# Kernel optimization log

Measured on AMD Instinct MI355X. Metric: run time of the kernel, lower is better.

Reference implementation:

```python
import jax, jax.numpy as jnp
import numpy as np
from jax.scipy.special import erfinv

EMBED = 384
HEADS = 6
HEAD_DIM = EMBED // HEADS  # 64
N_FREQS = HEAD_DIM // 2    # 32
SEQ = 1025                 # 1 CLS + 32*32 patches
POS_DIM = 2
MIN_FREQ, MAX_FREQ = 0.1, 1000.0


def _phi(m: int) -> float:
    x = 2.0
    for _ in range(10):
        x = (1.0 + x) ** (1.0 / (m + 1.0))
    return x


def _uniform_directions(n: int, d: int) -> jnp.ndarray:
    # golden-ratio quasi-random directions, normalized (matches uniform_directions_jax)
    g = _phi(d)
    alpha = (1.0 / g) ** jnp.arange(1, d + 1, dtype=jnp.float32)
    i = jnp.arange(1, n + 1, dtype=jnp.float32)[:, None]
    z = jnp.fmod(i * alpha, 1.0)
    dirs = erfinv(2.0 * z - 1.0)
    return dirs / jnp.linalg.norm(dirs, axis=1, keepdims=True)


def _rope_freqs() -> jnp.ndarray:  # [h, F, P]
    omega = MIN_FREQ * (MAX_FREQ / MIN_FREQ) ** jnp.linspace(0.0, 1.0, N_FREQS)
    dirs = _uniform_directions(HEADS * N_FREQS, POS_DIM).reshape(HEADS, N_FREQS, POS_DIM)
    return dirs * omega.reshape(1, N_FREQS, 1)


def _coords_2d() -> jnp.ndarray:  # [S, 2], CLS at origin, patches in [-1,1]^2
    n = int(np.sqrt(SEQ - 1))  # 32
    yy, xx = jnp.meshgrid(jnp.arange(n), jnp.arange(n), indexing='ij')
    xf = xx.flatten().astype(jnp.float32) / (n - 1) * 2 - 1
    yf = yy.flatten().astype(jnp.float32) / (n - 1) * 2 - 1
    patch = jnp.stack([xf, yf], axis=1)
    return jnp.concatenate([jnp.zeros((1, 2), jnp.float32), patch], axis=0)


def _apply_rope(t_bshd, freqs_hFP, coords_SP):
    # theta: [S, h, F]
    theta = jnp.einsum('hfp,sp->shf', freqs_hFP, coords_SP)
    cos, sin = jnp.cos(theta), jnp.sin(theta)  # broadcast over batch
    x1, y1 = jnp.split(t_bshd, 2, axis=-1)     # [b,s,h,F] each
    return jnp.concatenate([x1 * cos - y1 * sin, x1 * sin + y1 * cos], axis=-1)


def setup_inputs() -> dict:
    key = jax.random.key(0)
    ks = jax.random.split(key, 6)
    scale = 1.0 / np.sqrt(EMBED)
    return {
        'x':  jax.random.normal(ks[0], (16, SEQ, EMBED), jnp.float32),
        'Wq': jax.random.normal(ks[1], (EMBED, EMBED), jnp.float32) * scale,
        'Wk': jax.random.normal(ks[2], (EMBED, EMBED), jnp.float32) * scale,
        'Wv': jax.random.normal(ks[3], (EMBED, EMBED), jnp.float32) * scale,
        'Wo': jax.random.normal(ks[4], (EMBED, EMBED), jnp.float32) * scale,
        'bo': jnp.zeros((EMBED,), jnp.float32),
    }


def reference(x, Wq, Wk, Wv, Wo, bo):
    b, s, e = x.shape
    freqs = _rope_freqs()   # constant buffers
    coords = _coords_2d()
    q = (x @ Wq).reshape(b, s, HEADS, HEAD_DIM)
    k = (x @ Wk).reshape(b, s, HEADS, HEAD_DIM)
    v = (x @ Wv).reshape(b, s, HEADS, HEAD_DIM)
    q = _apply_rope(q, freqs, coords)
    k = _apply_rope(k, freqs, coords)
    scores = jnp.einsum('blhd,bmhd->bhlm', q, k) / np.sqrt(HEAD_DIM)
    attn = jax.nn.softmax(scores, axis=-1)
    out = jnp.einsum('bhlm,bmhd->blhd', attn, v).reshape(b, s, e)
    return out @ Wo + bo
```

## Files before the change

kernel.cpp:

```cpp
#include <hip/hip_runtime.h>
#include <hip/hip_bf16.h>
#include <math.h>

#define EMBED 384
#define HEADS 6
#define HD    64
#define NF    32
#define SEQ   1025
#define SEQP  1088
#define BATCH 16
#define MTOT  (BATCH*SEQ)
#define NCHUNK 17
#define LSTRIDE 72
#define VSTR   68
#define GSTR 40

typedef __bf16 bf16x8 __attribute__((ext_vector_type(8)));
typedef __bf16 bf16x4 __attribute__((ext_vector_type(4)));
typedef float  f32x4  __attribute__((ext_vector_type(4)));
typedef short  s16x4  __attribute__((ext_vector_type(4)));

#define MFMA_BF16(A,B,C) __builtin_amdgcn_mfma_f32_16x16x32_bf16((A),(B),(C),0,0,0)
#define MFMA16(A,B,C) __builtin_amdgcn_mfma_f32_16x16x16bf16_1k((A),(B),(C),0,0,0)

__device__ __forceinline__ __bf16 f2bf(float f){
    __hip_bfloat16 h = __float2bfloat16(f);
    return *reinterpret_cast<__bf16*>(&h);
}
__device__ __forceinline__ short bfbits(float f){
    __hip_bfloat16 h = __float2bfloat16(f);
    return *reinterpret_cast<short*>(&h);
}

__global__ __launch_bounds__(256) void x_to_bf16_kernel(
    const float* __restrict__ x, __hip_bfloat16* __restrict__ xb)
{
    const int n4 = MTOT*EMBED/4;
    int i = blockIdx.x*256 + threadIdx.x;
    if (i < n4){
        float4 v = *reinterpret_cast<const float4*>(x + (size_t)i*4);
        bf16x4 b; b[0]=f2bf(v.x); b[1]=f2bf(v.y); b[2]=f2bf(v.z); b[3]=f2bf(v.w);
        *reinterpret_cast<bf16x4*>(reinterpret_cast<__bf16*>(xb) + (size_t)i*4) = b;
    }
}

__global__ __launch_bounds__(256) void transpose_w_kernel(
    const float* __restrict__ Wq, const float* __restrict__ Wk,
    const float* __restrict__ Wv, const float* __restrict__ Wo,
    __hip_bfloat16* __restrict__ Wt)
{
    __shared__ float tile[64][65];
    const int mat = blockIdx.z;
    const float* W = (mat==0)?Wq:(mat==1)?Wk:(mat==2)?Wv:Wo;
    const int k0 = blockIdx.x*64, n0 = blockIdx.y*64;
    const int c = threadIdx.x & 63, rq = threadIdx.x >> 6;
    #pragma unroll
    for (int i = 0; i < 16; ++i){
        int row = rq*16 + i;
        tile[row][c] = W[(size_t)(k0+row)*EMBED + n0 + c];
    }
    __syncthreads();
    #pragma unroll
    for (int i = 0; i < 16; ++i){
        int nr = rq*16 + i;
        Wt[((size_t)mat*EMBED + n0 + nr)*EMBED + k0 + c] = __float2bfloat16(tile[c][nr]);
    }
}

__device__ __forceinline__ float erfinv_f(float x){
    float w = -log1pf(-x*x);
    float p;
    if (w < 5.0f){
        w -= 2.5f;
        p = 2.81022636e-08f;
        p = fmaf(p, w, 3.43273939e-07f);
        p = fmaf(p, w, -3.5233877e-06f);
        p = fmaf(p, w, -4.39150654e-06f);
        p = fmaf(p, w, 0.00021858087f);
        p = fmaf(p, w, -0.00125372503f);
        p = fmaf(p, w, -0.00417768164f);
        p = fmaf(p, w, 0.246640727f);
        p = fmaf(p, w, 1.50140941f);
    } else {
        w = sqrtf(w) - 3.0f;
        p = -0.000200214257f;
        p = fmaf(p, w, 0.000100950558f);
        p = fmaf(p, w, 0.00134934322f);
        p = fmaf(p, w, -0.00367342844f);
        p = fmaf(p, w, 0.00573950773f);
        p = fmaf(p, w, -0.0076224613f);
        p = fmaf(p, w, 0.00943887047f);
        p = fmaf(p, w, 1.00167406f);
        p = fmaf(p, w, 2.83297682f);
    }
    return p * x;
}

__global__ void rope_tables_kernel(float* __restrict__ cos_t, float* __restrict__ sin_t){
    int idx = blockIdx.x * blockDim.x + threadIdx.x;
    if (idx >= SEQ*HEADS*NF) return;
    int f  = idx & (NF-1);
    int hf = idx / NF;
    int h  = hf % HEADS;
    int s  = hf / HEADS;

    double xd = 2.0;
    #pragma unroll
    for (int it = 0; it < 10; ++it) xd = cbrt(1.0 + xd);
    float a1 = (float)(1.0 / xd);
    float a2 = a1 * a1;

    float fi = (float)(h*NF + f + 1);
    float z1 = fmodf(fi * a1, 1.0f);
    float z2 = fmodf(fi * a2, 1.0f);
    float d1 = erfinv_f(2.0f*z1 - 1.0f);
    float d2 = erfinv_f(2.0f*z2 - 1.0f);
    float inv = 1.0f / sqrtf(d1*d1 + d2*d2);
    d1 *= inv; d2 *= inv;

    float omega = 0.1f * powf(10000.0f, (float)f / 31.0f);
    float fx = d1 * omega, fy = d2 * omega;

    float cx = 0.0f, cy = 0.0f;
    if (s > 0){
        int pi = s - 1;
        cx = (float)(pi & 31) / 31.0f * 2.0f - 1.0f;
        cy = (float)(pi >> 5) / 31.0f * 2.0f - 1.0f;
    }
    float theta = fx*cx + fy*cy;
    float sv, cv;
    sincosf(theta, &sv, &cv);
    cos_t[idx] = cv;
    sin_t[idx] = sv;
}

__global__ __launch_bounds__(256, 3) void qkv_rope_kernel(
    const __hip_bfloat16* __restrict__ xb_,
    const __hip_bfloat16* __restrict__ Wt,
    const float* __restrict__ cos_t,
    const float* __restrict__ sin_t,
    __hip_bfloat16* __restrict__ qbuf,
    __hip_bfloat16* __restrict__ kbuf,
    __hip_bfloat16* __restrict__ vbuf)
{
    __shared__ __align__(16) __bf16 xs[128*GSTR];
    __shared__ __align__(16) __bf16 bt[128*GSTR];
    const int tid = threadIdx.x;
    const int m0 = blockIdx.x * 128;
    const int j  = blockIdx.y;
    const __bf16* xb = reinterpret_cast<const __bf16*>(xb_);
    const __bf16* wt = reinterpret_cast<const __bf16*>(Wt);

    int soff[2], arow[2], brow[2];
    #pragma unroll
    for (int i = 0; i < 2; ++i){
        int g = tid + i*256;
        int row = g >> 2, kc = g & 3;
        soff[i] = row*GSTR + kc*8;
        int am = m0 + row; if (am > MTOT-1) am = MTOT-1;
        arow[i] = am;
        brow[i] = j*128 + row;
    }

    bf16x8 ar[2], br[2];
    #pragma unroll
    for (int i = 0; i < 2; ++i){
        int g = tid + i*256, kc = g & 3;
        ar[i] = *reinterpret_cast<const bf16x8*>(xb + (size_t)arow[i]*EMBED + kc*8);
        br[i] = *reinterpret_cast<const bf16x8*>(wt + (size_t)brow[i]*EMBED + kc*8);
    }

    const int w = tid >> 6;
    const int lane = tid & 63;
    const int quad = lane >> 4, low = lane & 15;
    const int mh = w >> 1, nh = w & 1;
    const int mw0 = m0 + mh*64;

    f32x4 acc[4][4] = {};
    for (int kb = 0; kb < 12; ++kb){
        __syncthreads();
        #pragma unroll
        for (int i = 0; i < 2; ++i){
            *reinterpret_cast<bf16x8*>(&xs[soff[i]]) = ar[i];
            *reinterpret_cast<bf16x8*>(&bt[soff[i]]) = br[i];
        }
        __syncthreads();
        if (kb < 11){
            const int k1 = (kb+1)*32;
            #pragma unroll
            for (int i = 0; i < 2; ++i){
                int g = tid + i*256, kc = g & 3;
                ar[i] = *reinterpret_cast<const bf16x8*>(xb + (size_t)arow[i]*EMBED + k1 + kc*8);
                br[i] = *reinterpret_cast<const bf16x8*>(wt + (size_t)brow[i]*EMBED + k1 + kc*8);
            }
        }
        bf16x8 af[4], bfr[4];
        #pragma unroll
        for (int mt = 0; mt < 4; ++mt)
            af[mt] = *reinterpret_cast<const bf16x8*>(&xs[(mh*64 + mt*16 + low)*GSTR + quad*8]);
        #pragma unroll
        for (int t = 0; t < 4; ++t)
            bfr[t] = *reinterpret_cast<const bf16x8*>(&bt[(nh*64 + t*16 + low)*GSTR + quad*8]);
        #pragma unroll
        for (int t = 0; t < 4; ++t)
            #pragma unroll
            for (int mt = 0; mt < 4; ++mt)
                acc[mt][t] = MFMA_BF16(af[mt], bfr[t], acc[mt][t]);
    }

    const int n64 = j*2 + nh;
    const int mat = n64 / 6;
    const int h   = n64 % 6;

    if (mat == 2){
        #pragma unroll
        for (int mt = 0; mt < 4; ++mt)
            #pragma unroll
            for (int t = 0; t < 4; ++t)
                #pragma unroll
                for (int r = 0; r < 4; ++r){
                    int m = mw0 + mt*16 + quad*4 + r;
                    if (m < MTOT){
                        int b = m / SEQ, s = m % SEQ;
                        vbuf[((size_t)(b*HEADS + h)*SEQ + s)*HD + t*16 + low] = __float2bfloat16(acc[mt][t][r]);
                    }
                }
    } else {
        __hip_bfloat16* ob = (mat == 0) ? qbuf : kbuf;
        const float qs_ = (mat == 0) ? 0.125f : 1.0f;
        #pragma unroll
        for (int mt = 0; mt < 4; ++mt)
            #pragma unroll
            for (int t = 0; t < 2; ++t)
                #pragma unroll
                for (int r = 0; r < 4; ++r){
                    int m = mw0 + mt*16 + quad*4 + r;
                    if (m < MTOT){
                        int b = m / SEQ, s = m % SEQ;
                        int f = t*16 + low;
                        float cv = cos_t[(s*HEADS + h)*NF + f];
                        float sv = sin_t[(s*HEADS + h)*NF + f];
                        float x1 = acc[mt][t][r];
                        float y1 = acc[mt][t+2][r];
                        size_t base = ((size_t)(b*HEADS + h)*SEQ + s)*HD;
                        ob[base + f]      = __float2bfloat16((x1*cv - y1*sv)*qs_);
                        ob[base + NF + f] = __float2bfloat16((x1*sv + y1*cv)*qs_);
                    }
                }
    }
}

__global__ __launch_bounds__(256) void vt_transpose_kernel(
    const __hip_bfloat16* __restrict__ v, __hip_bfloat16* __restrict__ vt)
{
    __shared__ __bf16 tileT[64*72];
    const int tid = threadIdx.x;
    const int bh = blockIdx.x;
    const int s0 = blockIdx.y * 64;
    const __bf16* vb = reinterpret_cast<const __bf16*>(v) + (size_t)bh*SEQ*HD;
    #pragma unroll
    for (int i = 0; i < 2; ++i){
        int ch = tid + i*256;
        int srow = ch >> 3, dg = ch & 7;
        int s = s0 + srow; if (s > SEQ-1) s = SEQ-1;
        bf16x8 val = *reinterpret_cast<const bf16x8*>(vb + (size_t)s*HD + dg*8);
        #pragma unroll
        for (int e = 0; e < 8; ++e)
            tileT[(dg*8 + e)*72 + srow] = val[e];
    }
    __syncthreads();
    __bf16* ot = reinterpret_cast<__bf16*>(vt) + (size_t)bh*HD*SEQP;
    #pragma unroll
    for (int i = 0; i < 2; ++i){
        int ch = tid + i*256;
        int d = ch >> 3, sg = ch & 7;
        bf16x8 val = *reinterpret_cast<const bf16x8*>(&tileT[d*72 + sg*8]);
        *reinterpret_cast<bf16x8*>(ot + (size_t)d*SEQP + s0 + sg*8) = val;
    }
}

__global__ __launch_bounds__(256, 4) void attn_kernel(
    const __hip_bfloat16* __restrict__ qbuf,
    const __hip_bfloat16* __restrict__ kbuf,
    const __hip_bfloat16* __restrict__ vtbuf,
    __hip_bfloat16* __restrict__ aout)
{
    __shared__ __align__(16) __bf16 kls[64*LSTRIDE];
    __shared__ __align__(16) __bf16 vls[64*VSTR];
    const int tid  = threadIdx.x;
    const int w    = tid >> 6;
    const int lane = tid & 63;
    const int quad = lane >> 4, low = lane & 15;
    const int id = blockIdx.x;
    const int bh = id % 96;
    const int qt = id / 96;
    const int b = bh / HEADS, h = bh % HEADS;
    const __bf16* qb = reinterpret_cast<const __bf16*>(qbuf);
    const __bf16* kb = reinterpret_cast<const __bf16*>(kbuf);
    const __bf16* vt = reinterpret_cast<const __bf16*>(vtbuf);
    const size_t base   = (size_t)bh * SEQ * HD;
    const size_t vtbase = (size_t)bh * HD * SEQP;
    const int q0 = qt*128 + w*32;

    int srow[2], sgk[2], soffk[2], soffv[2];
    #pragma unroll
    for (int i = 0; i < 2; ++i){
        int ch = tid + i*256;
        srow[i] = ch >> 3; sgk[i] = ch & 7;
        soffk[i] = srow[i]*LSTRIDE + sgk[i]*8;
        soffv[i] = srow[i]*VSTR    + sgk[i]*8;
    }

    bf16x8 bq[2][2];
    #pragma unroll
    for (int nt = 0; nt < 2; ++nt){
        int qs = q0 + nt*16 + low; if (qs > SEQ-1) qs = SEQ-1;
        #pragma unroll
        for (int ks = 0; ks < 2; ++ks)
            bq[nt][ks] = *reinterpret_cast<const bf16x8*>(qb + base + (size_t)qs*HD + ks*32 + quad*8);
    }

    bf16x8 kr[2], vr[2];
    #pragma unroll
    for (int i = 0; i < 2; ++i){
        int kk = srow[i]; if (kk > SEQ-1) kk = SEQ-1;
        kr[i] = *reinterpret_cast<const bf16x8*>(kb + base + (size_t)kk*HD + sgk[i]*8);
        vr[i] = *reinterpret_cast<const bf16x8*>(vt + vtbase + (size_t)srow[i]*SEQP + sgk[i]*8);
    }

    f32x4 o[2][4] = {};
    float l_i[2] = {0.f, 0.f};

    for (int c = 0; c < NCHUNK; ++c){
        const int c0 = c*64;
        __syncthreads();
        #pragma unroll
        for (int i = 0; i < 2; ++i){
            *reinterpret_cast<bf16x8*>(&kls[soffk[i]]) = kr[i];
            bf16x4 vlo = __builtin_shufflevector(vr[i], vr[i], 0,1,2,3);
            bf16x4 vhi = __builtin_shufflevector(vr[i], vr[i], 4,5,6,7);
            *reinterpret_cast<bf16x4*>(&vls[soffv[i]])     = vlo;
            *reinterpret_cast<bf16x4*>(&vls[soffv[i] + 4]) = vhi;
        }
        __syncthreads();
        if (c + 1 < NCHUNK){
            const int c1 = c0 + 64;
            #pragma unroll
            for (int i = 0; i < 2; ++i){
                int kk = c1 + srow[i]; if (kk > SEQ-1) kk = SEQ-1;
                kr[i] = *reinterpret_cast<const bf16x8*>(kb + base + (size_t)kk*HD + sgk[i]*8);
                vr[i] = *reinterpret_cast<const bf16x8*>(vt + vtbase + (size_t)srow[i]*SEQP + c1 + sgk[i]*8);
            }
        }
        f32x4 st[4][2] = {};
        #pragma unroll
        for (int kt = 0; kt < 4; ++kt)
            #pragma unroll
            for (int ks = 0; ks < 2; ++ks){
                bf16x8 ak = *reinterpret_cast<const bf16x8*>(&kls[(kt*16 + low)*LSTRIDE + ks*32 + quad*8]);
                #pragma unroll
                for (int nt = 0; nt < 2; ++nt)
                    st[kt][nt] = MFMA_BF16(ak, bq[nt][ks], st[kt][nt]);
            }
        if (c0 + 64 > SEQ){
            #pragma unroll
            for (int kt = 0; kt < 4; ++kt)
                #pragma unroll
                for (int r = 0; r < 4; ++r){
                    int key = c0 + kt*16 + quad*4 + r;
                    if (key >= SEQ){ st[kt][0][r] = -1e30f; st[kt][1][r] = -1e30f; }
                }
        }
        s16x4 pa[4][2];
        #pragma unroll
        for (int nt = 0; nt < 2; ++nt)
            #pragma unroll
            for (int kt = 0; kt < 4; ++kt)
                #pragma unroll
                for (int r = 0; r < 4; ++r){
                    float p = __expf(st[kt][nt][r]);
                    l_i[nt] += p;
                    pa[kt][nt][r] = bfbits(p);
                }
        #pragma unroll
        for (int kt = 0; kt < 4; ++kt)
            #pragma unroll
            for (int dt = 0; dt < 4; ++dt){
                const s16x4 bv = *reinterpret_cast<const s16x4*>(&vls[(dt*16 + low)*VSTR + kt*16 + quad*4]);
                #pragma unroll
                for (int nt = 0; nt < 2; ++nt)
                    o[nt][dt] = MFMA16(pa[kt][nt], bv, o[nt][dt]);
            }
    }

    #pragma unroll
    for (int nt = 0; nt < 2; ++nt){
        l_i[nt] += __shfl_xor(l_i[nt], 16, 64);
        l_i[nt] += __shfl_xor(l_i[nt], 32, 64);
    }
    float lq[2][4];
    #pragma unroll
    for (int nt = 0; nt < 2; ++nt)
        #pragma unroll
        for (int r = 0; r < 4; ++r)
            lq[nt][r] = __shfl(l_i[nt], quad*4 + r, 64);

    #pragma unroll
    for (int nt = 0; nt < 2; ++nt)
        #pragma unroll
        for (int r = 0; r < 4; ++r){
            int s = q0 + nt*16 + quad*4 + r;
            if (s < SEQ){
                float inv = 1.0f / lq[nt][r];
                __hip_bfloat16* dst = aout + ((size_t)b*SEQ + s)*EMBED + h*HD;
                #pragma unroll
                for (int dt = 0; dt < 4; ++dt)
                    dst[dt*16 + low] = __float2bfloat16(o[nt][dt][r]*inv);
            }
        }
}

__global__ __launch_bounds__(256, 3) void outproj_kernel(
    const __hip_bfloat16* __restrict__ a,
    const __hip_bfloat16* __restrict__ Wt,
    const float* __restrict__ bo,
    float* __restrict__ out)
{
    __shared__ __align__(16) __bf16 xs[128*GSTR];
    __shared__ __align__(16) __bf16 bt[128*GSTR];
    const int tid = threadIdx.x;
    const int m0 = blockIdx.x * 128;
    const int j  = blockIdx.y;
    const __bf16* ab = reinterpret_cast<const __bf16*>(a);
    const __bf16* wt = reinterpret_cast<const __bf16*>(Wt) + (size_t)3*EMBED*EMBED;

    int soff[2], arow[2], brow[2];
    #pragma unroll
    for (int i = 0; i < 2; ++i){
        int g = tid + i*256;
        int row = g >> 2, kc = g & 3;
        soff[i] = row*GSTR + kc*8;
        int am = m0 + row; if (am > MTOT-1) am = MTOT-1;
        arow[i] = am;
        brow[i] = j*128 + row;
    }
    bf16x8 ar[2], br[2];
    #pragma unroll
    for (int i = 0; i < 2; ++i){
        int g = tid + i*256, kc = g & 3;
        ar[i] = *reinterpret_cast<const bf16x8*>(ab + (size_t)arow[i]*EMBED + kc*8);
        br[i] = *reinterpret_cast<const bf16x8*>(wt + (size_t)brow[i]*EMBED + kc*8);
    }

    const int w = tid >> 6;
    const int lane = tid & 63;
    const int quad = lane >> 4, low = lane & 15;
    const int mh = w >> 1, nh = w & 1;
    const int mw0 = m0 + mh*64;
    const int n0 = j*128 + nh*64;

    f32x4 acc[4][4] = {};
    for (int kb = 0; kb < 12; ++kb){
        __syncthreads();
        #pragma unroll
        for (int i = 0; i < 2; ++i){
            *reinterpret_cast<bf16x8*>(&xs[soff[i]]) = ar[i];
            *reinterpret_cast<bf16x8*>(&bt[soff[i]]) = br[i];
        }
        __syncthreads();
        if (kb < 11){
            const int k1 = (kb+1)*32;
            #pragma unroll
            for (int i = 0; i < 2; ++i){
                int g = tid + i*256, kc = g & 3;
                ar[i] = *reinterpret_cast<const bf16x8*>(ab + (size_t)arow[i]*EMBED + k1 + kc*8);
                br[i] = *reinterpret_cast<const bf16x8*>(wt + (size_t)brow[i]*EMBED + k1 + kc*8);
            }
        }
        bf16x8 af[4], bfr[4];
        #pragma unroll
        for (int mt = 0; mt < 4; ++mt)
            af[mt] = *reinterpret_cast<const bf16x8*>(&xs[(mh*64 + mt*16 + low)*GSTR + quad*8]);
        #pragma unroll
        for (int t = 0; t < 4; ++t)
            bfr[t] = *reinterpret_cast<const bf16x8*>(&bt[(nh*64 + t*16 + low)*GSTR + quad*8]);
        #pragma unroll
        for (int t = 0; t < 4; ++t)
            #pragma unroll
            for (int mt = 0; mt < 4; ++mt)
                acc[mt][t] = MFMA_BF16(af[mt], bfr[t], acc[mt][t]);
    }

    #pragma unroll
    for (int t = 0; t < 4; ++t){
        const int n = n0 + t*16 + low;
        const float bias = bo[n];
        #pragma unroll
        for (int mt = 0; mt < 4; ++mt)
            #pragma unroll
            for (int r = 0; r < 4; ++r){
                const int m = mw0 + mt*16 + quad*4 + r;
                if (m < MTOT) out[(size_t)m*EMBED + n] = acc[mt][t][r] + bias;
            }
    }
}

extern "C" void kernel_launch(void* const* d_in, const int* in_sizes, int n_in,
                              void* d_out, int out_size, void* d_ws, size_t ws_size,
                              hipStream_t stream)
{
    const float* x  = (const float*)d_in[0];
    const float* Wq = (const float*)d_in[1];
    const float* Wk = (const float*)d_in[2];
    const float* Wv = (const float*)d_in[3];
    const float* Wo = (const float*)d_in[4];
    const float* bo = (const float*)d_in[5];
    float* out = (float*)d_out;

    const size_t NE = (size_t)MTOT * EMBED;
    const size_t VT = (size_t)BATCH*HEADS*HD*SEQP;
    char* ws = (char*)d_ws;
    size_t off = 0;
    __hip_bfloat16* qbuf = (__hip_bfloat16*)(ws + off); off += 2*NE;
    __hip_bfloat16* kbuf = (__hip_bfloat16*)(ws + off); off += 2*NE;
    __hip_bfloat16* abuf = (__hip_bfloat16*)(ws + off); off += 2*NE;
    __hip_bfloat16* vbuf = (__hip_bfloat16*)(ws + off); off += 2*NE;
    __hip_bfloat16* xbuf = (__hip_bfloat16*)(ws + off); off += 2*NE;
    __hip_bfloat16* vt   = (__hip_bfloat16*)(ws + off); off += 2*VT;
    __hip_bfloat16* Wt   = (__hip_bfloat16*)(ws + off); off += (size_t)4*EMBED*EMBED*2;
    float* cos_t = (float*)(ws + off); off += (size_t)SEQ*HEADS*NF*4;
    float* sin_t = (float*)(ws + off); off += (size_t)SEQ*HEADS*NF*4;

    x_to_bf16_kernel<<<dim3((MTOT*EMBED/4 + 255)/256), dim3(256), 0, stream>>>(x, xbuf);
    transpose_w_kernel<<<dim3(6,6,4), dim3(256), 0, stream>>>(Wq, Wk, Wv, Wo, Wt);
    rope_tables_kernel<<<dim3((SEQ*HEADS*NF + 255)/256), dim3(256), 0, stream>>>(cos_t, sin_t);
    qkv_rope_kernel<<<dim3((MTOT + 127)/128, 9), dim3(256), 0, stream>>>(xbuf, Wt, cos_t, sin_t, qbuf, kbuf, vbuf);
    vt_transpose_kernel<<<dim3(96, 17), dim3(256), 0, stream>>>(vbuf, vt);
    attn_kernel<<<dim3(864), dim3(256), 0, stream>>>(qbuf, kbuf, vt, abuf);
    outproj_kernel<<<dim3((MTOT + 127)/128, 3), dim3(256), 0, stream>>>(abuf, Wt, bo, out);
}
```

Measured before the change: 206.6 us.

## Handle the single leftover query row per head with a lightweight scalar block

Before, the attention grid padded SEQ=1025 to nine 128-row query tiles, so a whole ninth tile per (batch,head) existed only to compute row 1024. Now 768 heavy blocks cover rows 0..1023 with the bounds clamps and checks removed, and 96 light blocks each compute the final row with scalar dot products, exp2 and a reduction over the untransposed V. The log2(e) factor is folded into the Q scale so both paths use exp2f instead of expf. The light path is scalar and serial over 1025 keys, which could make it a straggler at the end of the launch.

```diff
diff --git a/kernel.cpp b/kernel.cpp
--- a/kernel.cpp
+++ b/kernel.cpp
@@ -14,6 +14,7 @@
 #define LSTRIDE 72
 #define VSTR   68
 #define GSTR 40
+#define NHEAVY 768
 
 typedef __bf16 bf16x8 __attribute__((ext_vector_type(8)));
 typedef __bf16 bf16x4 __attribute__((ext_vector_type(4)));
@@ -30,6 +31,11 @@
 __device__ __forceinline__ short bfbits(float f){
     __hip_bfloat16 h = __float2bfloat16(f);
     return *reinterpret_cast<short*>(&h);
+}
+__device__ __forceinline__ float bf2f(__bf16 b){
+    unsigned short u = __builtin_bit_cast(unsigned short, b);
+    unsigned int x = (unsigned int)u << 16;
+    return __builtin_bit_cast(float, x);
 }
 
 __global__ __launch_bounds__(256) void x_to_bf16_kernel(
@@ -227,7 +233,7 @@
                 }
     } else {
         __hip_bfloat16* ob = (mat == 0) ? qbuf : kbuf;
-        const float qs_ = (mat == 0) ? 0.125f : 1.0f;
+        const float qs_ = (mat == 0) ? 0.125f*1.44269504088896340736f : 1.0f;
         #pragma unroll
         for (int mt = 0; mt < 4; ++mt)
             #pragma unroll
@@ -283,6 +289,7 @@
     const __hip_bfloat16* __restrict__ qbuf,
     const __hip_bfloat16* __restrict__ kbuf,
     const __hip_bfloat16* __restrict__ vtbuf,
+    const __hip_bfloat16* __restrict__ vbuf,
     __hip_bfloat16* __restrict__ aout)
 {
     __shared__ __align__(16) __bf16 kls[64*LSTRIDE];
@@ -290,8 +297,53 @@
     const int tid  = threadIdx.x;
     const int w    = tid >> 6;
     const int lane = tid & 63;
+    const int id = blockIdx.x;
+
+    if (id >= NHEAVY){
+        const int bh = id - NHEAVY;
+        const int b = bh / HEADS, h = bh % HEADS;
+        const __bf16* qr = reinterpret_cast<const __bf16*>(qbuf) + ((size_t)bh*SEQ + 1024)*HD;
+        const __bf16* kb = reinterpret_cast<const __bf16*>(kbuf) + (size_t)bh*SEQ*HD;
+        const __bf16* vb = reinterpret_cast<const __bf16*>(vbuf) + (size_t)bh*SEQ*HD;
+        float* pbuf = reinterpret_cast<float*>(kls);
+        float* lred = pbuf + 1056;
+        float* ored = reinterpret_cast<float*>(vls);
+        float lsum = 0.f;
+        for (int k = tid; k < SEQ; k += 256){
+            float s = 0.f;
+            #pragma unroll
+            for (int dg = 0; dg < 8; ++dg){
+                bf16x8 k8 = *reinterpret_cast<const bf16x8*>(kb + (size_t)k*HD + dg*8);
+                bf16x8 q8 = *reinterpret_cast<const bf16x8*>(qr + dg*8);
+                #pragma unroll
+                for (int e = 0; e < 8; ++e)
+                    s = fmaf(bf2f(q8[e]), bf2f(k8[e]), s);
+            }
+            float p = exp2f(s);
+            pbuf[k] = p;
+            lsum += p;
+        }
+        #pragma unroll
+        for (int off = 32; off; off >>= 1) lsum += __shfl_xor(lsum, off, 64);
+        if (lane == 0) lred[w] = lsum;
+        __syncthreads();
+        const float ltot = lred[0] + lred[1] + lred[2] + lred[3];
+        const int kbeg = w*256;
+        const int kend = (w == 3) ? SEQ : kbeg + 256;
+        float osum = 0.f;
+        #pragma unroll 4
+        for (int k = kbeg; k < kend; ++k)
+            osum = fmaf(pbuf[k], bf2f(vb[(size_t)k*HD + lane]), osum);
+        ored[w*64 + lane] = osum;
+        __syncthreads();
+        if (tid < 64){
+            float o = ored[tid] + ored[64+tid] + ored[128+tid] + ored[192+tid];
+            aout[((size_t)b*SEQ + 1024)*EMBED + h*HD + tid] = __float2bfloat16(o / ltot);
+        }
+        return;
+    }
+
     const int quad = lane >> 4, low = lane & 15;
-    const int id = blockIdx.x;
     const int bh = id % 96;
     const int qt = id / 96;
     const int b = bh / HEADS, h = bh % HEADS;
@@ -314,7 +366,7 @@
     bf16x8 bq[2][2];
     #pragma unroll
     for (int nt = 0; nt < 2; ++nt){
-        int qs = q0 + nt*16 + low; if (qs > SEQ-1) qs = SEQ-1;
+        int qs = q0 + nt*16 + low;
         #pragma unroll
         for (int ks = 0; ks < 2; ++ks)
             bq[nt][ks] = *reinterpret_cast<const bf16x8*>(qb + base + (size_t)qs*HD + ks*32 + quad*8);
@@ -378,7 +430,7 @@
             for (int kt = 0; kt < 4; ++kt)
                 #pragma unroll
                 for (int r = 0; r < 4; ++r){
-                    float p = __expf(st[kt][nt][r]);
+                    float p = exp2f(st[kt][nt][r]);
                     l_i[nt] += p;
                     pa[kt][nt][r] = bfbits(p);
                 }
@@ -410,13 +462,11 @@
         #pragma unroll
         for (int r = 0; r < 4; ++r){
             int s = q0 + nt*16 + quad*4 + r;
-            if (s < SEQ){
-                float inv = 1.0f / lq[nt][r];
-                __hip_bfloat16* dst = aout + ((size_t)b*SEQ + s)*EMBED + h*HD;
-                #pragma unroll
-                for (int dt = 0; dt < 4; ++dt)
-                    dst[dt*16 + low] = __float2bfloat16(o[nt][dt][r]*inv);
-            }
+            float inv = 1.0f / lq[nt][r];
+            __hip_bfloat16* dst = aout + ((size_t)b*SEQ + s)*EMBED + h*HD;
+            #pragma unroll
+            for (int dt = 0; dt < 4; ++dt)
+                dst[dt*16 + low] = __float2bfloat16(o[nt][dt][r]*inv);
         }
 }
 
@@ -536,6 +586,6 @@
     rope_tables_kernel<<<dim3((SEQ*HEADS*NF + 255)/256), dim3(256), 0, stream>>>(cos_t, sin_t);
     qkv_rope_kernel<<<dim3((MTOT + 127)/128, 9), dim3(256), 0, stream>>>(xbuf, Wt, cos_t, sin_t, qbuf, kbuf, vbuf);
     vt_transpose_kernel<<<dim3(96, 17), dim3(256), 0, stream>>>(vbuf, vt);
-    attn_kernel<<<dim3(864), dim3(256), 0, stream>>>(qbuf, kbuf, vt, abuf);
+    attn_kernel<<<dim3(NHEAVY + 96), dim3(256), 0, stream>>>(qbuf, kbuf, vt, vbuf, abuf);
     outproj_kernel<<<dim3((MTOT + 127)/128, 3), dim3(256), 0, stream>>>(abuf, Wt, bo, out);
 }
```

Result: no change. 208.0 us (+0.7%).
